# Kernel tuning notes

Hardware: AMD Instinct MI355X
Metric: run time of the kernel (lower is better)

Reference implementation:

```python
import jax, jax.numpy as jnp
import numpy as np

DECAY = 0.999
EPS = 1e-05


def setup_inputs() -> dict:
    key = jax.random.key(0)
    k1, k2 = jax.random.split(key)
    B, L, S, D, E = 32, 8, 512, 256, 2048
    x = jax.random.normal(k1, (B, L, S, D), dtype=jnp.float32)
    # stacked per-quantizer codebooks: embed[l] is the [dim, n_embed] buffer of Quantize l
    embed = jax.random.normal(k2, (L, D, E), dtype=jnp.float32)
    cluster_size = jnp.zeros((L, E), dtype=jnp.float32)
    embed_avg = embed.copy()
    return {"x": x, "embed": embed, "cluster_size": cluster_size, "embed_avg": embed_avg}


def reference(x, embed, cluster_size, embed_avg):
    # x: [B, L, S, D]; embed: [L, D, E]; cluster_size: [L, E]; embed_avg: [L, D, E]
    B, L, S, D = x.shape
    E = embed.shape[-1]

    dist = ((x * x).sum(-1, keepdims=True)
            - 2.0 * jnp.einsum('blsd,lde->blse', x, embed)
            + (embed * embed).sum(1)[None, :, None, :])
    ids = jnp.argmin(dist, axis=-1)  # argmax of -dist == argmin of dist; [B, L, S]

    # codebook lookup: embed_t[l, ids[b,l,s]] -> [B, L, S, D]
    embed_t = jnp.swapaxes(embed, 1, 2)  # [L, E, D]
    q = embed_t[jnp.arange(L)[None, :, None], ids]

    # EMA buffer updates (training mode; done on .data in torch, i.e. no grad)
    l_idx = jnp.broadcast_to(jnp.arange(L)[None, :, None], (B, L, S))
    counts = jnp.zeros((L, E), x.dtype).at[l_idx, ids].add(1.0)  # onehot.sum(0) per quantizer
    embed_sum = jnp.zeros((L, E, D), x.dtype).at[l_idx, ids].add(jax.lax.stop_gradient(x))
    embed_sum = jnp.swapaxes(embed_sum, 1, 2)  # [L, D, E] == flatten.T @ onehot
    new_cluster_size = DECAY * cluster_size + (1.0 - DECAY) * counts
    new_embed_avg = DECAY * embed_avg + (1.0 - DECAY) * embed_sum
    n = new_cluster_size.sum(-1, keepdims=True)  # [L, 1]
    cs = (new_cluster_size + EPS) / (n + E * EPS) * n
    new_embed = new_embed_avg / cs[:, None, :]

    # NOTE: the original loop overwrites `diff` each iteration then does `diff += diff`,
    # so the returned diff is 2 * diff_of_last_quantizer / length (faithfully reproduced).
    diff_last = jnp.mean((jax.lax.stop_gradient(q[:, L - 1]) - x[:, L - 1]) ** 2)
    diff = 2.0 * diff_last / L

    # straight-through estimator
    out = x + jax.lax.stop_gradient(q - x)
    return out, diff, ids, new_embed, new_cluster_size, new_embed_avg
```

## Files before the change

### kernel.cpp

```cpp
#include <hip/hip_runtime.h>

#define LL 8
#define BB 32
#define SS 512
#define DD 256
#define EE 2048
#define LED (LL*DD*EE)
#define LE  (LL*EE)
#define NROWS (BB*LL*SS)
#define NKS 17

typedef __bf16 bf16x8 __attribute__((ext_vector_type(8)));
typedef float  f32x16 __attribute__((ext_vector_type(16)));

__global__ void transpose_norms_kernel(const float* __restrict__ embed,
                                       float* __restrict__ embed_t,
                                       float* __restrict__ norms) {
    __shared__ float tile[32][33];
    const int l  = blockIdx.z;
    const int d0 = blockIdx.y * 32;
    const int e0 = blockIdx.x * 32;
    const int tx = threadIdx.x, ty = threadIdx.y;

    float v = embed[((size_t)l*DD + d0 + ty)*EE + e0 + tx];
    tile[ty][tx] = v;
    __syncthreads();
    embed_t[((size_t)l*EE + e0 + ty)*DD + d0 + tx] = tile[tx][ty];
    __syncthreads();
    tile[ty][tx] = v * v;
    __syncthreads();
    if (ty == 0) {
        float s = 0.f;
        #pragma unroll
        for (int i = 0; i < 32; ++i) s += tile[i][tx];
        atomicAdd(&norms[l*EE + e0 + tx], s);
    }
}

__global__ void prep_embed_frag(const float* __restrict__ embed,
                                const float* __restrict__ norms,
                                __bf16* __restrict__ frag) {
    const int bid   = blockIdx.x;
    const int kstep = bid % NKS;
    const int mtile = (bid / NKS) % 64;
    const int l     = bid / (NKS * 64);
    const int lane  = threadIdx.x;
    const int e     = mtile*32 + (lane & 31);
    const int kbase = kstep*16 + (lane >> 5)*8;

    bf16x8 vh, vl;
    if (kstep < 16) {
        #pragma unroll
        for (int j = 0; j < 8; ++j) {
            float v = embed[((size_t)l*DD + kbase + j)*EE + e];
            __bf16 h = (__bf16)v;
            vh[j] = h;
            vl[j] = (__bf16)(v - (float)h);
        }
    } else {
        #pragma unroll
        for (int j = 0; j < 8; ++j) { vh[j] = (__bf16)0.0f; vl[j] = (__bf16)0.0f; }
        if (kbase == 256) {
            float nv = -0.5f * norms[l*EE + e];
            __bf16 ch = (__bf16)nv;
            vh[0] = ch;
            vh[1] = (__bf16)(nv - (float)ch);
        }
    }
    size_t base = ((((size_t)l*64 + mtile)*2 + 0)*NKS + kstep)*64 + lane;
    *(bf16x8*)(frag + base*8) = vh;
    base = ((((size_t)l*64 + mtile)*2 + 1)*NKS + kstep)*64 + lane;
    *(bf16x8*)(frag + base*8) = vl;
}

__global__ __launch_bounds__(256, 2)
void argmin_mfma(const float* __restrict__ x,
                 const __bf16* __restrict__ frag,
                 int* __restrict__ ids_out,
                 int* __restrict__ counts_i) {
    __shared__ __bf16 smem[2][2*NKS*512];

    const int tid  = threadIdx.x;
    const int wave = tid >> 6, lane = tid & 63;
    const int l    = blockIdx.x & 7;
    const int rb   = blockIdx.x >> 3;
    const int idx  = rb*4 + wave;
    const int b    = idx >> 4, st = idx & 15;
    const int rowtile = (b*LL + l)*16 + st;

    bf16x8 bh[NKS], bl[NKS];
    {
        const float* xr = x + (size_t)(rowtile*32 + (lane & 31))*DD + (lane >> 5)*8;
        #pragma unroll
        for (int ks = 0; ks < 16; ++ks) {
            float4 v0 = *(const float4*)(xr + ks*16);
            float4 v1 = *(const float4*)(xr + ks*16 + 4);
            float f[8] = {v0.x, v0.y, v0.z, v0.w, v1.x, v1.y, v1.z, v1.w};
            #pragma unroll
            for (int j = 0; j < 8; ++j) {
                __bf16 h = (__bf16)f[j];
                bh[ks][j] = h;
                bl[ks][j] = (__bf16)(f[j] - (float)h);
            }
        }
        #pragma unroll
        for (int j = 0; j < 8; ++j) { bh[16][j] = (__bf16)0.0f; bl[16][j] = (__bf16)0.0f; }
        if (lane < 32) { bh[16][0] = (__bf16)1.0f; bh[16][1] = (__bf16)1.0f; }
    }

    const __bf16* fl = frag + (size_t)l*64*2*NKS*512;

    auto stage = [&](int m, int buf) {
        const __bf16* src = fl + (size_t)m*2*NKS*512;
        __bf16* dst = &smem[buf][0];
        for (int i = wave; i < 2*NKS; i += 4) {
            __builtin_amdgcn_global_load_lds(
                (const __attribute__((address_space(1))) void*)(src + i*512 + lane*8),
                (__attribute__((address_space(3))) void*)(dst + i*512), 16, 0, 0);
        }
    };

    float maxv = -3.4e38f;
    int   maxi = 0;

    stage(0, 0);
    __syncthreads();
    for (int m = 0; m < 64; ++m) {
        const int buf = m & 1;
        if (m < 63) stage(m + 1, buf ^ 1);
        const __bf16* sA = &smem[buf][0];
        f32x16 acc;
        #pragma unroll
        for (int i = 0; i < 16; ++i) acc[i] = 0.0f;
        #pragma unroll
        for (int ks = 0; ks < NKS; ++ks) {
            bf16x8 ah = *(const bf16x8*)(sA + ks*512 + lane*8);
            bf16x8 al = *(const bf16x8*)(sA + (NKS + ks)*512 + lane*8);
            acc = __builtin_amdgcn_mfma_f32_32x32x16_bf16(ah, bh[ks], acc, 0, 0, 0);
            acc = __builtin_amdgcn_mfma_f32_32x32x16_bf16(ah, bl[ks], acc, 0, 0, 0);
            acc = __builtin_amdgcn_mfma_f32_32x32x16_bf16(al, bh[ks], acc, 0, 0, 0);
        }
        #pragma unroll
        for (int r = 0; r < 16; ++r) {
            int e = m*32 + (r & 3) + 8*(r >> 2) + 4*(lane >> 5);
            float v = acc[r];
            if (v > maxv || (v == maxv && e < maxi)) { maxv = v; maxi = e; }
        }
        __syncthreads();
    }
    float ov = __shfl_xor(maxv, 32, 64);
    int   oi = __shfl_xor(maxi, 32, 64);
    if (ov > maxv || (ov == maxv && oi < maxi)) { maxv = ov; maxi = oi; }
    if (lane < 32) {
        ids_out[(size_t)rowtile*32 + lane] = maxi;
        atomicAdd(&counts_i[l*EE + maxi], 1);
    }
}

__global__ __launch_bounds__(256)
void scan_kernel(const int* __restrict__ counts_i,
                 int* __restrict__ bin_start,
                 int* __restrict__ cursor) {
    __shared__ int part[256];
    const int l = blockIdx.x, tid = threadIdx.x;
    const int base = l*EE + tid*8;
    int local[8], tsum = 0;
    #pragma unroll
    for (int j = 0; j < 8; ++j) { local[j] = counts_i[base + j]; tsum += local[j]; }
    part[tid] = tsum;
    __syncthreads();
    for (int off = 1; off < 256; off <<= 1) {
        int v = (tid >= off) ? part[tid - off] : 0;
        __syncthreads();
        part[tid] += v;
        __syncthreads();
    }
    int run = part[tid] - tsum;
    #pragma unroll
    for (int j = 0; j < 8; ++j) {
        bin_start[base + j] = run;
        cursor[base + j]    = run;
        run += local[j];
    }
}

__global__ __launch_bounds__(256)
void scatter_idx_kernel(const int* __restrict__ ids,
                        int* __restrict__ cursor,
                        int* __restrict__ sorted_rows) {
    const int r = blockIdx.x*256 + threadIdx.x;
    const int l = (r >> 9) & 7;
    const int e = ids[r];
    int pos = atomicAdd(&cursor[l*EE + e], 1);
    sorted_rows[l*(NROWS/LL) + pos] = r;
}

__global__ __launch_bounds__(256)
void segsum_kernel(const float* __restrict__ x,
                   const int* __restrict__ sorted_rows,
                   const int* __restrict__ bin_start,
                   const int* __restrict__ counts_i,
                   float* __restrict__ embed_sum) {
    const int bid = blockIdx.x;
    const int l   = bid >> 11;
    const int e   = bid & 2047;
    const int tid = threadIdx.x;
    const int start = bin_start[l*EE + e];
    const int cnt   = counts_i[l*EE + e];
    const int* rows = sorted_rows + l*(NROWS/LL);

    float acc = 0.f;
    int i = 0;
    for (; i + 1 < cnt; i += 2) {
        int r0 = rows[start + i], r1 = rows[start + i + 1];
        acc += x[(size_t)r0*DD + tid] + x[(size_t)r1*DD + tid];
    }
    if (i < cnt) acc += x[(size_t)rows[start + i]*DD + tid];
    embed_sum[((size_t)l*EE + e)*DD + tid] = acc;
}

__global__ __launch_bounds__(256)
void gather_out_kernel(const float* __restrict__ x,
                       const float* __restrict__ embed_t,
                       const int* __restrict__ ids,
                       float* __restrict__ out,
                       float* __restrict__ diff_acc) {
    const int tid  = threadIdx.x;
    const size_t rf = (size_t)blockIdx.x*4 + (tid >> 6);
    const int lane = tid & 63;
    const int l    = (int)((rf >> 9) & 7);
    const int id   = ids[rf];

    float4 qv = ((const float4*)embed_t)[((size_t)l*EE + id)*64 + lane];
    ((float4*)out)[rf*64 + lane] = qv;

    if (l == LL - 1) {
        float4 xv = ((const float4*)x)[rf*64 + lane];
        float dx = qv.x - xv.x, dy = qv.y - xv.y, dz = qv.z - xv.z, dw = qv.w - xv.w;
        float sq = dx*dx + dy*dy + dz*dz + dw*dw;
        #pragma unroll
        for (int off = 32; off; off >>= 1) sq += __shfl_down(sq, off);
        __shared__ float wsum[4];
        if (lane == 0) wsum[tid >> 6] = sq;
        __syncthreads();
        if (tid == 0) atomicAdd(diff_acc, wsum[0] + wsum[1] + wsum[2] + wsum[3]);
    }
}

__global__ void finalize_cluster_kernel(const float* __restrict__ cs_in,
                                        const int* __restrict__ counts_i,
                                        float* __restrict__ ncs_out,
                                        float* __restrict__ n_out) {
    const int l = blockIdx.x, tid = threadIdx.x;
    float s = 0.f;
    for (int e = tid; e < EE; e += 256) {
        float v = 0.999f*cs_in[l*EE + e] + 0.001f*(float)counts_i[l*EE + e];
        ncs_out[l*EE + e] = v;
        s += v;
    }
    #pragma unroll
    for (int off = 32; off; off >>= 1) s += __shfl_down(s, off);
    __shared__ float red[4];
    if ((tid & 63) == 0) red[tid >> 6] = s;
    __syncthreads();
    if (tid == 0) n_out[l] = red[0] + red[1] + red[2] + red[3];
}

__global__ void finalize_embed_kernel(const float* __restrict__ embed_avg,
                                      const float* __restrict__ embed_sum,
                                      const float* __restrict__ ncs,
                                      const float* __restrict__ n,
                                      float* __restrict__ nea_out,
                                      float* __restrict__ ne_out) {
    __shared__ float tile[32][33];
    const int l  = blockIdx.z;
    const int d0 = blockIdx.y * 32;
    const int e0 = blockIdx.x * 32;
    const int tx = threadIdx.x, ty = threadIdx.y;

    tile[ty][tx] = embed_sum[((size_t)l*EE + e0 + ty)*DD + d0 + tx];
    __syncthreads();
    const size_t idx = ((size_t)l*DD + d0 + ty)*EE + e0 + tx;
    float nea = 0.999f*embed_avg[idx] + 0.001f*tile[tx][ty];
    nea_out[idx] = nea;
    float nl = n[l];
    float c  = ncs[l*EE + e0 + tx];
    float cs = (c + 1e-5f) / (nl + 0.02048f) * nl;
    ne_out[idx] = nea / cs;
}

__global__ void diff_scale_kernel(const float* __restrict__ diff_acc,
                                  float* __restrict__ diff_out) {
    *diff_out = (*diff_acc / (float)(BB*SS*DD)) * 0.25f;
}

extern "C" void kernel_launch(void* const* d_in, const int* in_sizes, int n_in,
                              void* d_out, int out_size, void* d_ws, size_t ws_size,
                              hipStream_t stream) {
    const float* x            = (const float*)d_in[0];
    const float* embed        = (const float*)d_in[1];
    const float* cluster_size = (const float*)d_in[2];
    const float* embed_avg    = (const float*)d_in[3];

    float* out      = (float*)d_out;
    float* diff_out = out + 33554432;
    int*   ids_out  = (int*)(out + 33554433);
    float* ne_out   = out + 33685505;
    float* ncs_out  = out + 37879809;
    float* nea_out  = out + 37896193;

    float* ws        = (float*)d_ws;
    float* embed_t   = ws;
    float* embed_sum = ws + LED;
    int*   counts_i  = (int*)(ws + 2*(size_t)LED);
    float* norms     = ws + 2*(size_t)LED + LE;
    float* diff_acc  = norms + LE;
    float* n_ws      = diff_acc + 1;
    int*   bin_start = (int*)(n_ws + LL);
    int*   cursor    = bin_start + LE;
    int*   sorted_rows = cursor + LE;
    __bf16* embfrag  = (__bf16*)(sorted_rows + NROWS + 16);

    hipMemsetAsync(counts_i, 0, (size_t)(2*LE + 1) * sizeof(float), stream);

    transpose_norms_kernel<<<dim3(EE/32, DD/32, LL), dim3(32, 32), 0, stream>>>(
        embed, embed_t, norms);

    prep_embed_frag<<<LL*64*NKS, 64, 0, stream>>>(embed, norms, embfrag);

    argmin_mfma<<<1024, 256, 0, stream>>>(x, embfrag, ids_out, counts_i);

    scan_kernel<<<LL, 256, 0, stream>>>(counts_i, bin_start, cursor);

    scatter_idx_kernel<<<NROWS/256, 256, 0, stream>>>(ids_out, cursor, sorted_rows);

    segsum_kernel<<<LE, 256, 0, stream>>>(x, sorted_rows, bin_start, counts_i, embed_sum);

    gather_out_kernel<<<NROWS/4, 256, 0, stream>>>(x, embed_t, ids_out, out, diff_acc);

    finalize_cluster_kernel<<<LL, 256, 0, stream>>>(cluster_size, counts_i, ncs_out, n_ws);

    finalize_embed_kernel<<<dim3(EE/32, DD/32, LL), dim3(32, 32), 0, stream>>>(
        embed_avg, embed_sum, ncs_out, n_ws, nea_out, ne_out);

    diff_scale_kernel<<<1, 1, 0, stream>>>(diff_acc, diff_out);
}
```

Baseline: 934.4 us.

## Fuse codebook gather into argmin kernel and split MFMA accumulator chains

New measurement: 960.1 us. 1.03x slower.

```diff
diff --git a/kernel.cpp b/kernel.cpp
--- a/kernel.cpp
+++ b/kernel.cpp
@@ -76,8 +76,11 @@
 __global__ __launch_bounds__(256, 2)
 void argmin_mfma(const float* __restrict__ x,
                  const __bf16* __restrict__ frag,
+                 const float* __restrict__ embed_t,
                  int* __restrict__ ids_out,
-                 int* __restrict__ counts_i) {
+                 int* __restrict__ counts_i,
+                 float* __restrict__ out,
+                 float* __restrict__ diff_acc) {
     __shared__ __bf16 smem[2][2*NKS*512];
 
     const int tid  = threadIdx.x;
@@ -88,7 +91,7 @@
     const int b    = idx >> 4, st = idx & 15;
     const int rowtile = (b*LL + l)*16 + st;
 
-    bf16x8 bh[NKS], bl[NKS];
+    bf16x8 bh[NKS], bl[16];
     {
         const float* xr = x + (size_t)(rowtile*32 + (lane & 31))*DD + (lane >> 5)*8;
         #pragma unroll
@@ -104,7 +107,7 @@
             }
         }
         #pragma unroll
-        for (int j = 0; j < 8; ++j) { bh[16][j] = (__bf16)0.0f; bl[16][j] = (__bf16)0.0f; }
+        for (int j = 0; j < 8; ++j) bh[16][j] = (__bf16)0.0f;
         if (lane < 32) { bh[16][0] = (__bf16)1.0f; bh[16][1] = (__bf16)1.0f; }
     }
 
@@ -129,22 +132,27 @@
         const int buf = m & 1;
         if (m < 63) stage(m + 1, buf ^ 1);
         const __bf16* sA = &smem[buf][0];
-        f32x16 acc;
-        #pragma unroll
-        for (int i = 0; i < 16; ++i) acc[i] = 0.0f;
-        #pragma unroll
-        for (int ks = 0; ks < NKS; ++ks) {
+        f32x16 a0, a1, a2;
+        #pragma unroll
+        for (int i = 0; i < 16; ++i) { a0[i] = 0.0f; a1[i] = 0.0f; a2[i] = 0.0f; }
+        #pragma unroll
+        for (int ks = 0; ks < 16; ++ks) {
             bf16x8 ah = *(const bf16x8*)(sA + ks*512 + lane*8);
             bf16x8 al = *(const bf16x8*)(sA + (NKS + ks)*512 + lane*8);
-            acc = __builtin_amdgcn_mfma_f32_32x32x16_bf16(ah, bh[ks], acc, 0, 0, 0);
-            acc = __builtin_amdgcn_mfma_f32_32x32x16_bf16(ah, bl[ks], acc, 0, 0, 0);
-            acc = __builtin_amdgcn_mfma_f32_32x32x16_bf16(al, bh[ks], acc, 0, 0, 0);
-        }
+            a0 = __builtin_amdgcn_mfma_f32_32x32x16_bf16(ah, bh[ks], a0, 0, 0, 0);
+            a1 = __builtin_amdgcn_mfma_f32_32x32x16_bf16(ah, bl[ks], a1, 0, 0, 0);
+            a2 = __builtin_amdgcn_mfma_f32_32x32x16_bf16(al, bh[ks], a2, 0, 0, 0);
+        }
+        {
+            bf16x8 ah = *(const bf16x8*)(sA + 16*512 + lane*8);
+            a0 = __builtin_amdgcn_mfma_f32_32x32x16_bf16(ah, bh[16], a0, 0, 0, 0);
+        }
+        const int ebase = m*32 + 4*(lane >> 5);
         #pragma unroll
         for (int r = 0; r < 16; ++r) {
-            int e = m*32 + (r & 3) + 8*(r >> 2) + 4*(lane >> 5);
-            float v = acc[r];
-            if (v > maxv || (v == maxv && e < maxi)) { maxv = v; maxi = e; }
+            float v = a0[r] + a1[r] + a2[r];
+            int e = ebase + (r & 3) + 8*(r >> 2);
+            if (v > maxv) { maxv = v; maxi = e; }
         }
         __syncthreads();
     }
@@ -155,18 +163,51 @@
         ids_out[(size_t)rowtile*32 + lane] = maxi;
         atomicAdd(&counts_i[l*EE + maxi], 1);
     }
+
+    const float4* et4  = (const float4*)embed_t;
+    const float4* x4   = (const float4*)x;
+    float4*       out4 = (float4*)out;
+    float sq = 0.f;
+    #pragma unroll 4
+    for (int r = 0; r < 32; ++r) {
+        int id = __shfl(maxi, r);
+        float4 qv = et4[((size_t)l*EE + id)*64 + lane];
+        size_t o = ((size_t)rowtile*32 + r)*64 + lane;
+        out4[o] = qv;
+        if (l == LL - 1) {
+            float4 xv = x4[o];
+            float dx = qv.x - xv.x, dy = qv.y - xv.y, dz = qv.z - xv.z, dw = qv.w - xv.w;
+            sq += dx*dx + dy*dy + dz*dz + dw*dw;
+        }
+    }
+    if (l == LL - 1) {
+        #pragma unroll
+        for (int off = 32; off; off >>= 1) sq += __shfl_down(sq, off);
+        if (lane == 0) atomicAdd(diff_acc, sq);
+    }
 }
 
 __global__ __launch_bounds__(256)
 void scan_kernel(const int* __restrict__ counts_i,
+                 const float* __restrict__ cs_in,
                  int* __restrict__ bin_start,
-                 int* __restrict__ cursor) {
+                 int* __restrict__ cursor,
+                 float* __restrict__ ncs_out,
+                 float* __restrict__ n_out) {
     __shared__ int part[256];
+    __shared__ float red[4];
     const int l = blockIdx.x, tid = threadIdx.x;
     const int base = l*EE + tid*8;
     int local[8], tsum = 0;
+    float fsum = 0.f;
     #pragma unroll
-    for (int j = 0; j < 8; ++j) { local[j] = counts_i[base + j]; tsum += local[j]; }
+    for (int j = 0; j < 8; ++j) {
+        local[j] = counts_i[base + j];
+        tsum += local[j];
+        float v = 0.999f*cs_in[base + j] + 0.001f*(float)local[j];
+        ncs_out[base + j] = v;
+        fsum += v;
+    }
     part[tid] = tsum;
     __syncthreads();
     for (int off = 1; off < 256; off <<= 1) {
@@ -182,6 +223,11 @@
         cursor[base + j]    = run;
         run += local[j];
     }
+    #pragma unroll
+    for (int off = 32; off; off >>= 1) fsum += __shfl_down(fsum, off);
+    if ((tid & 63) == 0) red[tid >> 6] = fsum;
+    __syncthreads();
+    if (tid == 0) n_out[l] = red[0] + red[1] + red[2] + red[3];
 }
 
 __global__ __launch_bounds__(256)
@@ -219,53 +265,6 @@
     embed_sum[((size_t)l*EE + e)*DD + tid] = acc;
 }
 
-__global__ __launch_bounds__(256)
-void gather_out_kernel(const float* __restrict__ x,
-                       const float* __restrict__ embed_t,
-                       const int* __restrict__ ids,
-                       float* __restrict__ out,
-                       float* __restrict__ diff_acc) {
-    const int tid  = threadIdx.x;
-    const size_t rf = (size_t)blockIdx.x*4 + (tid >> 6);
-    const int lane = tid & 63;
-    const int l    = (int)((rf >> 9) & 7);
-    const int id   = ids[rf];
-
-    float4 qv = ((const float4*)embed_t)[((size_t)l*EE + id)*64 + lane];
-    ((float4*)out)[rf*64 + lane] = qv;
-
-    if (l == LL - 1) {
-        float4 xv = ((const float4*)x)[rf*64 + lane];
-        float dx = qv.x - xv.x, dy = qv.y - xv.y, dz = qv.z - xv.z, dw = qv.w - xv.w;
-        float sq = dx*dx + dy*dy + dz*dz + dw*dw;
-        #pragma unroll
-        for (int off = 32; off; off >>= 1) sq += __shfl_down(sq, off);
-        __shared__ float wsum[4];
-        if (lane == 0) wsum[tid >> 6] = sq;
-        __syncthreads();
-        if (tid == 0) atomicAdd(diff_acc, wsum[0] + wsum[1] + wsum[2] + wsum[3]);
-    }
-}
-
-__global__ void finalize_cluster_kernel(const float* __restrict__ cs_in,
-                                        const int* __restrict__ counts_i,
-                                        float* __restrict__ ncs_out,
-                                        float* __restrict__ n_out) {
-    const int l = blockIdx.x, tid = threadIdx.x;
-    float s = 0.f;
-    for (int e = tid; e < EE; e += 256) {
-        float v = 0.999f*cs_in[l*EE + e] + 0.001f*(float)counts_i[l*EE + e];
-        ncs_out[l*EE + e] = v;
-        s += v;
-    }
-    #pragma unroll
-    for (int off = 32; off; off >>= 1) s += __shfl_down(s, off);
-    __shared__ float red[4];
-    if ((tid & 63) == 0) red[tid >> 6] = s;
-    __syncthreads();
-    if (tid == 0) n_out[l] = red[0] + red[1] + red[2] + red[3];
-}
-
 __global__ void finalize_embed_kernel(const float* __restrict__ embed_avg,
                                       const float* __restrict__ embed_sum,
                                       const float* __restrict__ ncs,
@@ -328,17 +327,15 @@
 
     prep_embed_frag<<<LL*64*NKS, 64, 0, stream>>>(embed, norms, embfrag);
 
-    argmin_mfma<<<1024, 256, 0, stream>>>(x, embfrag, ids_out, counts_i);
-
-    scan_kernel<<<LL, 256, 0, stream>>>(counts_i, bin_start, cursor);
+    argmin_mfma<<<1024, 256, 0, stream>>>(x, embfrag, embed_t, ids_out, counts_i,
+                                          out, diff_acc);
+
+    scan_kernel<<<LL, 256, 0, stream>>>(counts_i, cluster_size, bin_start, cursor,
+                                        ncs_out, n_ws);
 
     scatter_idx_kernel<<<NROWS/256, 256, 0, stream>>>(ids_out, cursor, sorted_rows);
 
     segsum_kernel<<<LE, 256, 0, stream>>>(x, sorted_rows, bin_start, counts_i, embed_sum);
-
-    gather_out_kernel<<<NROWS/4, 256, 0, stream>>>(x, embed_t, ids_out, out, diff_acc);
-
-    finalize_cluster_kernel<<<LL, 256, 0, stream>>>(cluster_size, counts_i, ncs_out, n_ws);
 
     finalize_embed_kernel<<<dim3(EE/32, DD/32, LL), dim3(32, 32), 0, stream>>>(
         embed_avg, embed_sum, ncs_out, n_ws, nea_out, ne_out);
```
